# Kernel tuning notes

Measured on AMD Instinct MI355X. Metric: run time of the kernel, lower is better.

The kernel has to match this reference:

```python
import jax, jax.numpy as jnp
import numpy as np

N = 50000   # num_node
E = 1600000 # edge_size (N * avg_degree 32)
B = 64      # batch, hardcoded via repeat(64,1,1) in the torch module


def setup_inputs() -> dict:
    key = jax.random.key(0)
    k = jax.random.split(key, 8)
    return {
        "t": jax.random.normal(k[0], (1,), dtype=jnp.float32),
        "input": jax.random.normal(k[1], (B, N), dtype=jnp.float32),
        "edge_i": jax.random.randint(k[2], (E,), 0, N, dtype=jnp.int32),
        "edge_j": jax.random.randint(k[3], (E,), 0, N, dtype=jnp.int32),
        "weight_react": jax.random.normal(k[4], (1, E), dtype=jnp.float32) / 10.0,
        "weight_diff": jax.random.normal(k[5], (1, E), dtype=jnp.float32) / 1000.0,
        "bias_reaction": jax.random.normal(k[6], (1, N), dtype=jnp.float32) / 10.0,
        "bias_diffusion": jax.random.normal(k[7], (1, N), dtype=jnp.float32) / 10.0,
    }


def _lap_matvec(x, w, src, dst, n):
    # W[src_e, dst_e] = w_e (duplicates coalesce by sum, as torch sparse_coo_tensor does)
    # L = diag(colsum(W)) - W ; returns x @ L^T applied batched: out[b, v] = (L x[b])[v]
    col = jax.ops.segment_sum(w, dst, num_segments=n)                 # [N] column sums
    msg = jax.ops.segment_sum(w[:, None] * x[:, dst].T, src,
                              num_segments=n)                          # [N, B]
    return col[None, :] * x - msg.T                                   # [B, N]


def reference(t, input, edge_i, edge_j, weight_react, weight_diff,
              bias_reaction, bias_diffusion):
    x = input                                                          # [B, N]
    n = x.shape[1]
    # reaction Laplacian uses edges (i -> j); diffusion uses transposed (j -> i)
    reaction = _lap_matvec(x, weight_react[0], edge_i, edge_j, n) + bias_reaction
    diffusion = _lap_matvec(x, weight_diff[0], edge_j, edge_i, n) + bias_diffusion
    # up and down both True: tanh(reaction) + diffusion + input
    return jnp.tanh(reaction) + diffusion + x
```

## Files before the change

kernel.cpp:

```cpp
#include <hip/hip_runtime.h>
#include <hip/hip_fp16.h>


#define BKT_SHIFT 7
#define BKT_NODES 128
#define RCAP 4608
#define RCAP2 4992
#define CH 4096
#define NBP 512

#define RFL(x) __builtin_amdgcn_readfirstlane(x)

__device__ __forceinline__ unsigned bf16_rne(float f) {
    unsigned u = __float_as_uint(f);
    unsigned rb = (u >> 16) & 1u;
    u += 0x7FFFu + rb;
    return u >> 16;
}
__device__ __forceinline__ float bf16_lo(int y) {
    return __uint_as_float(((unsigned)y) << 16);
}

__global__ void zero_kernel(float4* __restrict__ p, int n4) {
    int i = blockIdx.x * blockDim.x + threadIdx.x;
    int s = gridDim.x * blockDim.x;
    float4 z = make_float4(0.f, 0.f, 0.f, 0.f);
    for (; i < n4; i += s) p[i] = z;
}

__global__ void transpose_kernel(const float* __restrict__ x, __half* __restrict__ xth, int N) {
    __shared__ float tile[64][65];
    int v0 = blockIdx.x * 64;
    int tx = threadIdx.x;
    int ty = threadIdx.y;
    if (v0 + tx < N) {
        for (int b = ty; b < 64; b += 16)
            tile[tx][b] = x[b * N + v0 + tx];
    }
    __syncthreads();
    for (int vl = ty; vl < 64; vl += 16) {
        int v = v0 + vl;
        if (v < N)
            xth[(size_t)v * 64 + tx] = __float2half(tile[vl][tx]);
    }
}

__global__ void __launch_bounds__(512) partition_kernel(
        const int* __restrict__ ei, const int* __restrict__ ej,
        const float* __restrict__ wr, const float* __restrict__ wd,
        int* __restrict__ gcur, int2* __restrict__ runs,
        int E, int NB) {
    __shared__ int cnt[2 * NBP];
    __shared__ int base_a[2 * NBP];
    __shared__ int gb[2 * NBP];
    __shared__ int2 buf[2 * CH];

    int tid = threadIdx.x;
    int e0 = blockIdx.x * CH;
    int ch_len = min(CH, E - e0);
    if (ch_len <= 0) return;

    for (int b = tid; b < 2 * NBP; b += 512) cnt[b] = 0;
    __syncthreads();
    for (int t = tid; t < ch_len; t += 512) {
        int i = ei[e0 + t], j = ej[e0 + t];
        atomicAdd(&cnt[i >> BKT_SHIFT], 1);
        atomicAdd(&cnt[NBP + (j >> BKT_SHIFT)], 1);
    }
    __syncthreads();
    if (tid < 64) {
        int carry = 0;
        #pragma unroll
        for (int c = 0; c < (2 * NBP) / 64; ++c) {
            int idx = c * 64 + tid;
            int val = cnt[idx];
            int scan = val;
            for (int off = 1; off < 64; off <<= 1) {
                int n = __shfl_up(scan, off, 64);
                if (tid >= off) scan += n;
            }
            int excl = scan - val + carry;
            base_a[idx] = excl;
            cnt[idx] = excl;
            carry += __shfl(scan, 63, 64);
        }
    }
    __syncthreads();
    for (int t = tid; t < ch_len; t += 512) {
        int e = e0 + t;
        int i = ei[e], j = ej[e];
        float wrv = wr[e], wdv = wd[e];
        unsigned br16 = bf16_rne(wrv), bd16 = bf16_rne(wdv);
        int b0 = i >> BKT_SHIFT;
        int p0 = atomicAdd(&cnt[b0], 1);
        buf[p0] = make_int2((int)(((unsigned)b0 << 23) | ((unsigned)(i & 127) << 16) | (unsigned)j),
                            (int)((br16 << 16) | bd16));
        int b1 = j >> BKT_SHIFT;
        int p1 = atomicAdd(&cnt[NBP + b1], 1);
        buf[p1] = make_int2((int)(((unsigned)b1 << 23) | ((unsigned)(j & 127) << 16) | (unsigned)i),
                            (int)((bd16 << 16) | br16));
    }
    __syncthreads();
    for (int cb = tid; cb < 2 * NBP; cb += 512) {
        int n = cnt[cb] - base_a[cb];
        if (n > 0) {
            int side = cb >> 9;
            int bkt = cb & (NBP - 1);
            gb[cb] = atomicAdd(&gcur[side * NB + bkt], n);
        }
    }
    __syncthreads();
    int total = 2 * ch_len;
    for (int t = tid; t < total; t += 512) {
        int2 p = buf[t];
        int side = (t >= ch_len) ? 1 : 0;
        int bkt = ((unsigned)p.x >> 23) & 0x1FF;
        int cb = side * NBP + bkt;
        int rank = gb[cb] + (t - base_a[cb]);
        if (rank < RCAP)
            runs[((size_t)(side * NB + bkt)) * RCAP + rank] = p;
    }
}

__global__ void __launch_bounds__(512) csr_kernel(
        const int* __restrict__ gcur, const int2* __restrict__ runs,
        int* __restrict__ runs2, int4* __restrict__ meta, int NB, int N) {
    __shared__ int cnt[BKT_NODES];
    __shared__ int cur[BKT_NODES];
    __shared__ int pb[BKT_NODES];
    __shared__ float csum[BKT_NODES];
    __shared__ int src_c[RCAP];
    __shared__ unsigned char dlb[RCAP];
    __shared__ int dst[RCAP2];
    __shared__ int total_s;

    int sb = blockIdx.x;
    int side = (sb >= NB) ? 1 : 0;
    int b = sb - side * NB;
    int v0 = b << BKT_SHIFT;
    int len = min(gcur[sb], RCAP);
    size_t roff = (size_t)sb * RCAP;
    size_t roff2 = (size_t)sb * RCAP2;
    int tid = threadIdx.x;

    if (tid < BKT_NODES) { cnt[tid] = 0; csum[tid] = 0.f; }
    __syncthreads();
    for (int k = tid; k < len; k += 512) {
        int2 p = runs[roff + k];
        int dl = ((unsigned)p.x >> 16) & 0x7F;
        src_c[k] = (int)(((unsigned)p.y & 0xFFFF0000u) | ((unsigned)p.x & 0xFFFFu));
        dlb[k] = (unsigned char)dl;
        atomicAdd(&cnt[dl], 1);
        atomicAdd(&csum[dl], bf16_lo(p.y));
    }
    __syncthreads();
    if (tid < 64) {
        int carry = 0;
        #pragma unroll
        for (int c = 0; c < BKT_NODES / 64; ++c) {
            int idx = c * 64 + tid;
            int val = (cnt[idx] + 3) & ~3;
            int scan = val;
            for (int off = 1; off < 64; off <<= 1) {
                int n = __shfl_up(scan, off, 64);
                if (tid >= off) scan += n;
            }
            int excl = scan - val + carry;
            pb[idx] = excl;
            cur[idx] = excl;
            carry += __shfl(scan, 63, 64);
        }
        if (tid == 63) total_s = carry;
    }
    __syncthreads();
    if (tid < BKT_NODES) {
        int v = v0 + tid;
        if (v < N)
            meta[(size_t)side * N + v] =
                make_int4((int)(roff2 + pb[tid]), cnt[tid], __float_as_int(csum[tid]), 0);
        int pc = (cnt[tid] + 3) & ~3;
        for (int t = cnt[tid]; t < pc; ++t) dst[pb[tid] + t] = 0;
    }
    __syncthreads();
    for (int k = tid; k < len; k += 512) {
        int dl = dlb[k];
        int pos = atomicAdd(&cur[dl], 1);
        dst[pos] = src_c[k];
    }
    __syncthreads();
    int total = total_s;
    for (int k = tid; k < total; k += 512)
        runs2[roff2 + k] = dst[k];
}

__device__ __forceinline__ void pair_acc(int pA, int pB,
                                         const __half2* __restrict__ xth2,
                                         int halfl, bool hi, float2& acc) {
    int oA = RFL(pA) & 0xFFFF;
    int oB = RFL(pB) & 0xFFFF;
    float wA = __uint_as_float((unsigned)RFL(pA) & 0xFFFF0000u);
    float wB = __uint_as_float((unsigned)RFL(pB) & 0xFFFF0000u);
    int o = hi ? oB : oA;
    float w = hi ? wB : wA;
    float2 xf = __half22float2(xth2[((size_t)o << 5) + halfl]);
    acc.x = fmaf(w, xf.x, acc.x);
    acc.y = fmaf(w, xf.y, acc.y);
}

__global__ void __launch_bounds__(256) gather_kernel(
        const __half2* __restrict__ xth2, const int* __restrict__ runs2,
        const int4* __restrict__ meta,
        const float* __restrict__ br, const float* __restrict__ bd,
        float2* __restrict__ outt2, int N) {
    int lane = threadIdx.x & 63;
    int halfl = lane & 31;
    bool hi = lane >= 32;
    int v = blockIdx.x * 4 + (threadIdx.x >> 6);
    if (v >= N) return;
    int4 mr = meta[v];
    int4 md = meta[(size_t)N + v];
    int rbase = RFL(mr.x), rn = RFL(mr.y);
    int dbase = RFL(md.x), dn = RFL(md.y);
    float cold = __int_as_float(RFL(mr.z));
    float colr = __int_as_float(RFL(md.z));

    const int4* sr = (const int4*)(runs2 + rbase);
    const int4* sd = (const int4*)(runs2 + dbase);
    int nqr = (rn + 3) >> 2;
    int nqd = (dn + 3) >> 2;
    int nq = max(nqr, nqd);
    float2 accr = make_float2(0.f, 0.f);
    float2 accd = make_float2(0.f, 0.f);
    for (int q = 0; q < nq; ++q) {
        if (q < nqr) {
            int4 qa = sr[q];
            pair_acc(qa.x, qa.y, xth2, halfl, hi, accr);
            pair_acc(qa.z, qa.w, xth2, halfl, hi, accr);
        }
        if (q < nqd) {
            int4 qb = sd[q];
            pair_acc(qb.x, qb.y, xth2, halfl, hi, accd);
            pair_acc(qb.z, qb.w, xth2, halfl, hi, accd);
        }
    }
    accr.x += __shfl_xor(accr.x, 32);
    accr.y += __shfl_xor(accr.y, 32);
    accd.x += __shfl_xor(accd.x, 32);
    accd.y += __shfl_xor(accd.y, 32);

    float brv = br[v], bdv = bd[v];
    float2 xv = __half22float2(xth2[((size_t)v << 5) + halfl]);
    float r0 = colr * xv.x - accr.x + brv;
    float r1 = colr * xv.y - accr.y + brv;
    float d0 = cold * xv.x - accd.x + bdv;
    float d1 = cold * xv.y - accd.y + bdv;
    float2 res;
    res.x = tanhf(r0) + d0 + xv.x;
    res.y = tanhf(r1) + d1 + xv.y;
    if (!hi)
        outt2[((size_t)v << 5) + halfl] = res;
}

__global__ void transpose_out_kernel(const float* __restrict__ outt,
                                     float* __restrict__ out, int N) {
    __shared__ float tile[64][65];
    int v0 = blockIdx.x * 64;
    int tx = threadIdx.x;
    int ty = threadIdx.y;
    for (int vl = ty; vl < 64; vl += 16) {
        int v = v0 + vl;
        if (v < N)
            tile[vl][tx] = outt[(size_t)v * 64 + tx];
    }
    __syncthreads();
    if (v0 + tx < N) {
        for (int b = ty; b < 64; b += 16)
            out[b * N + v0 + tx] = tile[tx][b];
    }
}

extern "C" void kernel_launch(void* const* d_in, const int* in_sizes, int n_in,
                              void* d_out, int out_size, void* d_ws, size_t ws_size,
                              hipStream_t stream) {
    const float* x  = (const float*)d_in[1];
    const int*   ei = (const int*)d_in[2];
    const int*   ej = (const int*)d_in[3];
    const float* wr = (const float*)d_in[4];
    const float* wd = (const float*)d_in[5];
    const float* br = (const float*)d_in[6];
    const float* bd = (const float*)d_in[7];
    float* out = (float*)d_out;

    int E = in_sizes[2];
    int N = in_sizes[6];
    int NB = (N + BKT_NODES - 1) >> BKT_SHIFT;
    (void)out_size; (void)ws_size; (void)n_in;

    char* w = (char*)d_ws;
    float* outt = (float*)w;   w += (size_t)N * 64 * 4;
    __half* xth = (__half*)w;  w += (size_t)N * 64 * 2;
    int* gcur   = (int*)w;     w += (size_t)((2 * NB + 3) / 4) * 4 * 4;
    w = (char*)(((uintptr_t)w + 15) & ~(uintptr_t)15);
    int4* meta  = (int4*)w;    w += (size_t)2 * N * 16;
    int2* runs  = (int2*)w;    w += (size_t)2 * NB * RCAP * 8;
    int* runs2  = (int*)w;

    zero_kernel<<<4, 256, 0, stream>>>((float4*)gcur, (2 * NB + 3) / 4);

    dim3 tb(64, 16);
    int ntiles = (N + 63) / 64;
    transpose_kernel<<<ntiles, tb, 0, stream>>>(x, xth, N);

    int nchunks = (E + CH - 1) / CH;
    partition_kernel<<<nchunks, 512, 0, stream>>>(ei, ej, wr, wd, gcur, runs, E, NB);

    csr_kernel<<<2 * NB, 512, 0, stream>>>(gcur, runs, runs2, meta, NB, N);

    int gblocks = (N + 3) / 4;
    gather_kernel<<<gblocks, 256, 0, stream>>>((const __half2*)xth, runs2, meta,
                                               br, bd, (float2*)outt, N);

    transpose_out_kernel<<<ntiles, tb, 0, stream>>>(outt, out, N);
}
```

Measured before the change: 224.3 us.

## Fuse CSR build with gather and merge epilogue with output transpose

The per-bucket CSR kernel now performs the neighbour gather directly from its shared-memory sorted edge list, writing fp16 per-side messages and column sums. This removes the runs2/meta round trip through global memory and the separate gather kernel. A final kernel reads x directly, transposes the messages in LDS and applies the epilogue, which replaces the fp32 transposed output and its extra transpose pass. Zeroing of gcur is folded into the input transpose, and the partition kernel loads edges into registers once instead of twice. In exchange, the gather now runs on only about 782 blocks, each with 8 waves, which may lower parallelism, and messages are rounded to fp16.

```diff
diff --git a/kernel.cpp b/kernel.cpp
--- a/kernel.cpp
+++ b/kernel.cpp
@@ -20,19 +20,18 @@
 __device__ __forceinline__ float bf16_lo(int y) {
     return __uint_as_float(((unsigned)y) << 16);
 }
-
-__global__ void zero_kernel(float4* __restrict__ p, int n4) {
-    int i = blockIdx.x * blockDim.x + threadIdx.x;
-    int s = gridDim.x * blockDim.x;
-    float4 z = make_float4(0.f, 0.f, 0.f, 0.f);
-    for (; i < n4; i += s) p[i] = z;
-}
-
-__global__ void transpose_kernel(const float* __restrict__ x, __half* __restrict__ xth, int N) {
+__device__ __forceinline__ float bf16_hi(int y) {
+    return __uint_as_float((unsigned)y & 0xFFFF0000u);
+}
+
+__global__ void transpose_kernel(const float* __restrict__ x, __half* __restrict__ xth,
+                                 int* __restrict__ gcur, int ngcur, int N) {
     __shared__ float tile[64][65];
     int v0 = blockIdx.x * 64;
     int tx = threadIdx.x;
     int ty = threadIdx.y;
+    int flat = blockIdx.x * 1024 + ty * 64 + tx;
+    if (flat < ngcur) gcur[flat] = 0;
     if (v0 + tx < N) {
         for (int b = ty; b < 64; b += 16)
             tile[tx][b] = x[b * N + v0 + tx];
@@ -60,12 +59,29 @@
     int ch_len = min(CH, E - e0);
     if (ch_len <= 0) return;
 
+    int my_i[8], my_j[8];
+    unsigned my_w[8];
+    #pragma unroll
+    for (int k = 0; k < 8; ++k) {
+        int t = tid + k * 512;
+        if (t < ch_len) {
+            int e = e0 + t;
+            my_i[k] = ei[e];
+            my_j[k] = ej[e];
+            my_w[k] = (bf16_rne(wr[e]) << 16) | bf16_rne(wd[e]);
+        } else {
+            my_i[k] = -1;
+        }
+    }
+
     for (int b = tid; b < 2 * NBP; b += 512) cnt[b] = 0;
     __syncthreads();
-    for (int t = tid; t < ch_len; t += 512) {
-        int i = ei[e0 + t], j = ej[e0 + t];
-        atomicAdd(&cnt[i >> BKT_SHIFT], 1);
-        atomicAdd(&cnt[NBP + (j >> BKT_SHIFT)], 1);
+    #pragma unroll
+    for (int k = 0; k < 8; ++k) {
+        if (my_i[k] >= 0) {
+            atomicAdd(&cnt[my_i[k] >> BKT_SHIFT], 1);
+            atomicAdd(&cnt[NBP + (my_j[k] >> BKT_SHIFT)], 1);
+        }
     }
     __syncthreads();
     if (tid < 64) {
@@ -86,19 +102,20 @@
         }
     }
     __syncthreads();
-    for (int t = tid; t < ch_len; t += 512) {
-        int e = e0 + t;
-        int i = ei[e], j = ej[e];
-        float wrv = wr[e], wdv = wd[e];
-        unsigned br16 = bf16_rne(wrv), bd16 = bf16_rne(wdv);
-        int b0 = i >> BKT_SHIFT;
-        int p0 = atomicAdd(&cnt[b0], 1);
-        buf[p0] = make_int2((int)(((unsigned)b0 << 23) | ((unsigned)(i & 127) << 16) | (unsigned)j),
-                            (int)((br16 << 16) | bd16));
-        int b1 = j >> BKT_SHIFT;
-        int p1 = atomicAdd(&cnt[NBP + b1], 1);
-        buf[p1] = make_int2((int)(((unsigned)b1 << 23) | ((unsigned)(j & 127) << 16) | (unsigned)i),
-                            (int)((bd16 << 16) | br16));
+    #pragma unroll
+    for (int k = 0; k < 8; ++k) {
+        if (my_i[k] >= 0) {
+            int i = my_i[k], j = my_j[k];
+            unsigned wv = my_w[k];
+            int b0 = i >> BKT_SHIFT;
+            int p0 = atomicAdd(&cnt[b0], 1);
+            buf[p0] = make_int2((int)(((unsigned)b0 << 23) | ((unsigned)(i & 127) << 16) | (unsigned)j),
+                                (int)wv);
+            int b1 = j >> BKT_SHIFT;
+            int p1 = atomicAdd(&cnt[NBP + b1], 1);
+            buf[p1] = make_int2((int)(((unsigned)b1 << 23) | ((unsigned)(j & 127) << 16) | (unsigned)i),
+                                (int)((wv << 16) | (wv >> 16)));
+        }
     }
     __syncthreads();
     for (int cb = tid; cb < 2 * NBP; cb += 512) {
@@ -122,9 +139,11 @@
     }
 }
 
-__global__ void __launch_bounds__(512) csr_kernel(
+__global__ void __launch_bounds__(512) sortgather_kernel(
         const int* __restrict__ gcur, const int2* __restrict__ runs,
-        int* __restrict__ runs2, int4* __restrict__ meta, int NB, int N) {
+        const __half* __restrict__ xth,
+        __half* __restrict__ msg, float* __restrict__ colsum,
+        int NB, int N) {
     __shared__ int cnt[BKT_NODES];
     __shared__ int cur[BKT_NODES];
     __shared__ int pb[BKT_NODES];
@@ -132,7 +151,6 @@
     __shared__ int src_c[RCAP];
     __shared__ unsigned char dlb[RCAP];
     __shared__ int dst[RCAP2];
-    __shared__ int total_s;
 
     int sb = blockIdx.x;
     int side = (sb >= NB) ? 1 : 0;
@@ -140,7 +158,6 @@
     int v0 = b << BKT_SHIFT;
     int len = min(gcur[sb], RCAP);
     size_t roff = (size_t)sb * RCAP;
-    size_t roff2 = (size_t)sb * RCAP2;
     int tid = threadIdx.x;
 
     if (tid < BKT_NODES) { cnt[tid] = 0; csum[tid] = 0.f; }
@@ -170,14 +187,9 @@
             cur[idx] = excl;
             carry += __shfl(scan, 63, 64);
         }
-        if (tid == 63) total_s = carry;
     }
     __syncthreads();
     if (tid < BKT_NODES) {
-        int v = v0 + tid;
-        if (v < N)
-            meta[(size_t)side * N + v] =
-                make_int4((int)(roff2 + pb[tid]), cnt[tid], __float_as_int(csum[tid]), 0);
         int pc = (cnt[tid] + 3) & ~3;
         for (int t = cnt[tid]; t < pc; ++t) dst[pb[tid] + t] = 0;
     }
@@ -188,94 +200,88 @@
         dst[pos] = src_c[k];
     }
     __syncthreads();
-    int total = total_s;
-    for (int k = tid; k < total; k += 512)
-        runs2[roff2 + k] = dst[k];
-}
-
-__device__ __forceinline__ void pair_acc(int pA, int pB,
-                                         const __half2* __restrict__ xth2,
-                                         int halfl, bool hi, float2& acc) {
-    int oA = RFL(pA) & 0xFFFF;
-    int oB = RFL(pB) & 0xFFFF;
-    float wA = __uint_as_float((unsigned)RFL(pA) & 0xFFFF0000u);
-    float wB = __uint_as_float((unsigned)RFL(pB) & 0xFFFF0000u);
-    int o = hi ? oB : oA;
-    float w = hi ? wB : wA;
-    float2 xf = __half22float2(xth2[((size_t)o << 5) + halfl]);
-    acc.x = fmaf(w, xf.x, acc.x);
-    acc.y = fmaf(w, xf.y, acc.y);
-}
-
-__global__ void __launch_bounds__(256) gather_kernel(
-        const __half2* __restrict__ xth2, const int* __restrict__ runs2,
-        const int4* __restrict__ meta,
-        const float* __restrict__ br, const float* __restrict__ bd,
-        float2* __restrict__ outt2, int N) {
-    int lane = threadIdx.x & 63;
-    int halfl = lane & 31;
-    bool hi = lane >= 32;
-    int v = blockIdx.x * 4 + (threadIdx.x >> 6);
-    if (v >= N) return;
-    int4 mr = meta[v];
-    int4 md = meta[(size_t)N + v];
-    int rbase = RFL(mr.x), rn = RFL(mr.y);
-    int dbase = RFL(md.x), dn = RFL(md.y);
-    float cold = __int_as_float(RFL(mr.z));
-    float colr = __int_as_float(RFL(md.z));
-
-    const int4* sr = (const int4*)(runs2 + rbase);
-    const int4* sd = (const int4*)(runs2 + dbase);
-    int nqr = (rn + 3) >> 2;
-    int nqd = (dn + 3) >> 2;
-    int nq = max(nqr, nqd);
-    float2 accr = make_float2(0.f, 0.f);
-    float2 accd = make_float2(0.f, 0.f);
-    for (int q = 0; q < nq; ++q) {
-        if (q < nqr) {
-            int4 qa = sr[q];
-            pair_acc(qa.x, qa.y, xth2, halfl, hi, accr);
-            pair_acc(qa.z, qa.w, xth2, halfl, hi, accr);
-        }
-        if (q < nqd) {
-            int4 qb = sd[q];
-            pair_acc(qb.x, qb.y, xth2, halfl, hi, accd);
-            pair_acc(qb.z, qb.w, xth2, halfl, hi, accd);
-        }
-    }
-    accr.x += __shfl_xor(accr.x, 32);
-    accr.y += __shfl_xor(accr.y, 32);
-    accd.x += __shfl_xor(accd.x, 32);
-    accd.y += __shfl_xor(accd.y, 32);
-
-    float brv = br[v], bdv = bd[v];
-    float2 xv = __half22float2(xth2[((size_t)v << 5) + halfl]);
-    float r0 = colr * xv.x - accr.x + brv;
-    float r1 = colr * xv.y - accr.y + brv;
-    float d0 = cold * xv.x - accd.x + bdv;
-    float d1 = cold * xv.y - accd.y + bdv;
-    float2 res;
-    res.x = tanhf(r0) + d0 + xv.x;
-    res.y = tanhf(r1) + d1 + xv.y;
-    if (!hi)
-        outt2[((size_t)v << 5) + halfl] = res;
-}
-
-__global__ void transpose_out_kernel(const float* __restrict__ outt,
-                                     float* __restrict__ out, int N) {
-    __shared__ float tile[64][65];
+
+    int lane = tid & 63;
+    int wid = tid >> 6;
+    for (int t = 0; t < BKT_NODES / 8; ++t) {
+        int dl = wid * (BKT_NODES / 8) + t;
+        int v = v0 + dl;
+        if (v >= N) continue;
+        int base = pb[dl];
+        int n = cnt[dl];
+        int nq = (n + 3) >> 2;
+        const int4* quads = (const int4*)(dst + base);
+        float acc = 0.f;
+        int q = 0;
+        for (; q + 2 <= nq; q += 2) {
+            int4 qa = quads[q];
+            int4 qb = quads[q + 1];
+            int p0 = RFL(qa.x), p1 = RFL(qa.y), p2 = RFL(qa.z), p3 = RFL(qa.w);
+            int p4 = RFL(qb.x), p5 = RFL(qb.y), p6 = RFL(qb.z), p7 = RFL(qb.w);
+            float x0 = __half2float(xth[((size_t)(p0 & 0xFFFF) << 6) + lane]);
+            float x1 = __half2float(xth[((size_t)(p1 & 0xFFFF) << 6) + lane]);
+            float x2 = __half2float(xth[((size_t)(p2 & 0xFFFF) << 6) + lane]);
+            float x3 = __half2float(xth[((size_t)(p3 & 0xFFFF) << 6) + lane]);
+            float x4 = __half2float(xth[((size_t)(p4 & 0xFFFF) << 6) + lane]);
+            float x5 = __half2float(xth[((size_t)(p5 & 0xFFFF) << 6) + lane]);
+            float x6 = __half2float(xth[((size_t)(p6 & 0xFFFF) << 6) + lane]);
+            float x7 = __half2float(xth[((size_t)(p7 & 0xFFFF) << 6) + lane]);
+            acc = fmaf(bf16_hi(p0), x0, acc);
+            acc = fmaf(bf16_hi(p1), x1, acc);
+            acc = fmaf(bf16_hi(p2), x2, acc);
+            acc = fmaf(bf16_hi(p3), x3, acc);
+            acc = fmaf(bf16_hi(p4), x4, acc);
+            acc = fmaf(bf16_hi(p5), x5, acc);
+            acc = fmaf(bf16_hi(p6), x6, acc);
+            acc = fmaf(bf16_hi(p7), x7, acc);
+        }
+        if (q < nq) {
+            int4 qa = quads[q];
+            int p0 = RFL(qa.x), p1 = RFL(qa.y), p2 = RFL(qa.z), p3 = RFL(qa.w);
+            float x0 = __half2float(xth[((size_t)(p0 & 0xFFFF) << 6) + lane]);
+            float x1 = __half2float(xth[((size_t)(p1 & 0xFFFF) << 6) + lane]);
+            float x2 = __half2float(xth[((size_t)(p2 & 0xFFFF) << 6) + lane]);
+            float x3 = __half2float(xth[((size_t)(p3 & 0xFFFF) << 6) + lane]);
+            acc = fmaf(bf16_hi(p0), x0, acc);
+            acc = fmaf(bf16_hi(p1), x1, acc);
+            acc = fmaf(bf16_hi(p2), x2, acc);
+            acc = fmaf(bf16_hi(p3), x3, acc);
+        }
+        msg[((size_t)side * N + v) * 64 + lane] = __float2half(acc);
+        if (lane == 0)
+            colsum[(size_t)side * N + v] = csum[dl];
+    }
+}
+
+__global__ void final_kernel(const float* __restrict__ x,
+                             const __half* __restrict__ msg,
+                             const float* __restrict__ colsum,
+                             const float* __restrict__ br, const float* __restrict__ bd,
+                             float* __restrict__ out, int N) {
+    __shared__ float tr[64][65];
+    __shared__ float td[64][65];
     int v0 = blockIdx.x * 64;
     int tx = threadIdx.x;
     int ty = threadIdx.y;
     for (int vl = ty; vl < 64; vl += 16) {
         int v = v0 + vl;
-        if (v < N)
-            tile[vl][tx] = outt[(size_t)v * 64 + tx];
-    }
-    __syncthreads();
-    if (v0 + tx < N) {
-        for (int b = ty; b < 64; b += 16)
-            out[b * N + v0 + tx] = tile[tx][b];
+        if (v < N) {
+            tr[vl][tx] = __half2float(msg[(size_t)v * 64 + tx]);
+            td[vl][tx] = __half2float(msg[((size_t)N + v) * 64 + tx]);
+        }
+    }
+    __syncthreads();
+    int v = v0 + tx;
+    if (v < N) {
+        float cold = colsum[v];
+        float colr = colsum[(size_t)N + v];
+        float brv = br[v], bdv = bd[v];
+        for (int b = ty; b < 64; b += 16) {
+            float xv = x[b * N + v];
+            float r = colr * xv - tr[tx][b] + brv;
+            float d = cold * xv - td[tx][b] + bdv;
+            out[b * N + v] = tanhf(r) + d + xv;
+        }
     }
 }
 
@@ -297,28 +303,21 @@
     (void)out_size; (void)ws_size; (void)n_in;
 
     char* w = (char*)d_ws;
-    float* outt = (float*)w;   w += (size_t)N * 64 * 4;
-    __half* xth = (__half*)w;  w += (size_t)N * 64 * 2;
-    int* gcur   = (int*)w;     w += (size_t)((2 * NB + 3) / 4) * 4 * 4;
+    __half* xth = (__half*)w;    w += (size_t)N * 64 * 2;
+    __half* msg = (__half*)w;    w += (size_t)2 * N * 64 * 2;
+    float* colsum = (float*)w;   w += (size_t)2 * N * 4;
+    int* gcur   = (int*)w;       w += (size_t)2 * NB * 4;
     w = (char*)(((uintptr_t)w + 15) & ~(uintptr_t)15);
-    int4* meta  = (int4*)w;    w += (size_t)2 * N * 16;
-    int2* runs  = (int2*)w;    w += (size_t)2 * NB * RCAP * 8;
-    int* runs2  = (int*)w;
-
-    zero_kernel<<<4, 256, 0, stream>>>((float4*)gcur, (2 * NB + 3) / 4);
+    int2* runs  = (int2*)w;
 
     dim3 tb(64, 16);
     int ntiles = (N + 63) / 64;
-    transpose_kernel<<<ntiles, tb, 0, stream>>>(x, xth, N);
+    transpose_kernel<<<ntiles, tb, 0, stream>>>(x, xth, gcur, 2 * NB, N);
 
     int nchunks = (E + CH - 1) / CH;
     partition_kernel<<<nchunks, 512, 0, stream>>>(ei, ej, wr, wd, gcur, runs, E, NB);
 
-    csr_kernel<<<2 * NB, 512, 0, stream>>>(gcur, runs, runs2, meta, NB, N);
-
-    int gblocks = (N + 3) / 4;
-    gather_kernel<<<gblocks, 256, 0, stream>>>((const __half2*)xth, runs2, meta,
-                                               br, bd, (float2*)outt, N);
-
-    transpose_out_kernel<<<ntiles, tb, 0, stream>>>(outt, out, N);
-}
+    sortgather_kernel<<<2 * NB, 512, 0, stream>>>(gcur, runs, xth, msg, colsum, NB, N);
+
+    final_kernel<<<ntiles, tb, 0, stream>>>(x, msg, colsum, br, bd, out, N);
+}
```

After: 229.7 us. 2.4% more time.
